# Kernel tuning notes

Hardware: AMD Instinct MI355X
Metric: run time of the kernel (lower is better)

The kernel has to match this reference:

```python
import jax, jax.numpy as jnp
import numpy as np

MU = 0.34
STD = 0.04
PATCH = 32
LOG_NORM_CONST = float(np.log(STD * np.sqrt(2.0 * np.pi)))


def _patch_means(unet_output, patch):
    # unet_output: [B, C, H, W] with B == 1 (original code implicitly requires it).
    B, C, H, W = unet_output.shape
    hp, wp = H // patch, W // patch
    x = unet_output.reshape(B * C, hp, patch, wp, patch)
    # mean over batch*channel and both intra-patch axes -> [hp, wp]
    return x.mean(axis=(0, 2, 4))


def reference(unet_output, transformer_output):
    means = _patch_means(unet_output, PATCH)              # [hp, wp]
    mask = transformer_output[0] >= 0.5                   # [hp, wp]

    # Positive branch: -log(pdf(mean) + 1e-6); original uses .item() -> detached,
    # so stop_gradient reproduces the (lack of) gradient through this branch.
    m_sg = jax.lax.stop_gradient(means)
    logpdf = -0.5 * jnp.square((m_sg - MU) / STD) - LOG_NORM_CONST
    pos_term = -jnp.log(jnp.exp(logpdf) + 1e-6)

    # Negative branch: MSE against zero = mean^2 (differentiable).
    neg_term = jnp.square(means)

    maskf = mask.astype(means.dtype)
    pos_cnt = jnp.sum(maskf)
    neg_cnt = jnp.sum(1.0 - maskf)
    positive_loss = jnp.sum(pos_term * maskf) / pos_cnt
    negative_loss = jnp.sum(neg_term * (1.0 - maskf)) / neg_cnt
    return positive_loss + negative_loss


def setup_inputs() -> dict:
    key = jax.random.key(0)
    k1, k2 = jax.random.split(key)
    unet_output = jax.random.uniform(k1, (1, 1, 8192, 8192), dtype=jnp.float32)
    transformer_output = jax.random.uniform(k2, (1, 256, 256), dtype=jnp.float32)
    return {"unet_output": unet_output, "transformer_output": transformer_output}
```

## Files before the change

### kernel.cpp

```cpp
#include <hip/hip_runtime.h>
#include <math.h>

#define IMG_H 8192
#define IMG_W 8192
#define PATCH 32
#define HP 256
#define WP 256
#define NPATCH (HP * WP)

__device__ __constant__ float c_MU  = 0.34f;
__device__ __constant__ float c_INV_STD = 25.0f;
__device__ __constant__ float c_LOG_NORM_CONST = -2.2999373f;

__global__ __launch_bounds__(256) void patch_mean_kernel(
    const float* __restrict__ x, float* __restrict__ means)
{
    const int wave  = threadIdx.x >> 6;
    const int lane  = threadIdx.x & 63;
    const int patch = blockIdx.x * 4 + wave;
    const int ph = patch >> 8;
    const int pw = patch & 255;

    const float* base = x + (size_t)(ph * PATCH) * IMG_W + (size_t)(pw * PATCH);
    const int r0 = lane >> 3;
    const int cv = lane & 7;

    float s = 0.0f;
#pragma unroll
    for (int i = 0; i < 4; ++i) {
        const float4 v = *reinterpret_cast<const float4*>(
            base + (size_t)(i * 8 + r0) * IMG_W + cv * 4);
        s += (v.x + v.y) + (v.z + v.w);
    }

#pragma unroll
    for (int off = 32; off >= 1; off >>= 1)
        s += __shfl_down(s, off, 64);

    if (lane == 0)
        means[patch] = s * (1.0f / 1024.0f);
}

__global__ __launch_bounds__(256) void loss_partial_kernel(
    const float* __restrict__ means, const float* __restrict__ tmask,
    float* __restrict__ acc)
{
    const int idx = (blockIdx.x * 256 + threadIdx.x) * 4;

    const float4 m4 = *reinterpret_cast<const float4*>(means + idx);
    const float4 t4 = *reinterpret_cast<const float4*>(tmask + idx);

    const float mv[4] = { m4.x, m4.y, m4.z, m4.w };
    const float tv[4] = { t4.x, t4.y, t4.z, t4.w };

    float pos = 0.0f, neg = 0.0f, cnt = 0.0f;
#pragma unroll
    for (int i = 0; i < 4; ++i) {
        const float z = (mv[i] - c_MU) * c_INV_STD;
        const float logpdf = -0.5f * z * z - c_LOG_NORM_CONST;
        const float pterm = -logf(expf(logpdf) + 1e-6f);
        const float nterm = mv[i] * mv[i];
        if (tv[i] >= 0.5f) { pos += pterm; cnt += 1.0f; }
        else               { neg += nterm; }
    }

#pragma unroll
    for (int off = 32; off >= 1; off >>= 1) {
        pos += __shfl_down(pos, off, 64);
        neg += __shfl_down(neg, off, 64);
        cnt += __shfl_down(cnt, off, 64);
    }

    __shared__ float s_pos[4], s_neg[4], s_cnt[4];
    const int wave = threadIdx.x >> 6;
    const int lane = threadIdx.x & 63;
    if (lane == 0) { s_pos[wave] = pos; s_neg[wave] = neg; s_cnt[wave] = cnt; }
    __syncthreads();

    if (threadIdx.x == 0) {
        float bp = s_pos[0] + s_pos[1] + s_pos[2] + s_pos[3];
        float bn = s_neg[0] + s_neg[1] + s_neg[2] + s_neg[3];
        float bc = s_cnt[0] + s_cnt[1] + s_cnt[2] + s_cnt[3];
        atomicAdd(&acc[0], bp);
        atomicAdd(&acc[1], bn);
        atomicAdd(&acc[2], bc);
    }
}

__global__ void finalize_kernel(const float* __restrict__ acc, float* __restrict__ out)
{
    const float pos_cnt = acc[2];
    const float neg_cnt = (float)NPATCH - pos_cnt;
    out[0] = acc[0] / pos_cnt + acc[1] / neg_cnt;
}

extern "C" void kernel_launch(void* const* d_in, const int* in_sizes, int n_in,
                              void* d_out, int out_size, void* d_ws, size_t ws_size,
                              hipStream_t stream)
{
    const float* unet  = (const float*)d_in[0];
    const float* trans = (const float*)d_in[1];
    float* out = (float*)d_out;

    float* means = (float*)d_ws;
    float* acc   = means + NPATCH;

    hipMemsetAsync(acc, 0, 3 * sizeof(float), stream);

    patch_mean_kernel<<<NPATCH / 4, 256, 0, stream>>>(unet, means);

    loss_partial_kernel<<<NPATCH / 1024, 256, 0, stream>>>(means, trans, acc);

    finalize_kernel<<<1, 1, 0, stream>>>(acc, out);
}
```

Measured before the change: 348.5 us.

## Fuse patch-mean and loss terms, replace atomics with single-block final reduction

The per-patch loss terms are now computed inside the patch-mean kernel, so the means array is no longer written and reread. Each block writes its partial sums to per-block slots, and a single 1024-thread kernel reduces them and computes the final loss. This drops the memset, the separate loss kernel and the atomics. The costs are an added syncthreads in the bandwidth-bound main kernel and a one-block tail reduction over 16K partials.

```diff
diff --git a/kernel.cpp b/kernel.cpp
--- a/kernel.cpp
+++ b/kernel.cpp
@@ -1,19 +1,15 @@
 #include <hip/hip_runtime.h>
 #include <math.h>
 
-#define IMG_H 8192
 #define IMG_W 8192
 #define PATCH 32
-#define HP 256
-#define WP 256
-#define NPATCH (HP * WP)
+#define NPATCH 65536
+#define NBLK   16384
 
-__device__ __constant__ float c_MU  = 0.34f;
-__device__ __constant__ float c_INV_STD = 25.0f;
-__device__ __constant__ float c_LOG_NORM_CONST = -2.2999373f;
-
-__global__ __launch_bounds__(256) void patch_mean_kernel(
-    const float* __restrict__ x, float* __restrict__ means)
+__global__ __launch_bounds__(256) void fused_patch_loss_kernel(
+    const float* __restrict__ x, const float* __restrict__ tmask,
+    float* __restrict__ p_pos, float* __restrict__ p_neg,
+    float* __restrict__ p_cnt)
 {
     const int wave  = threadIdx.x >> 6;
     const int lane  = threadIdx.x & 63;
@@ -37,31 +33,38 @@
     for (int off = 32; off >= 1; off >>= 1)
         s += __shfl_down(s, off, 64);
 
-    if (lane == 0)
-        means[patch] = s * (1.0f / 1024.0f);
+    __shared__ float s_pos[4], s_neg[4], s_cnt[4];
+    if (lane == 0) {
+        const float m = s * (1.0f / 1024.0f);
+        const float t = tmask[patch];
+        const float z = (m - 0.34f) * 25.0f;
+        const float logpdf = -0.5f * z * z + 2.2999373f;
+        const float pterm = -logf(expf(logpdf) + 1e-6f);
+        const float nterm = m * m;
+        const bool pos = (t >= 0.5f);
+        s_pos[wave] = pos ? pterm : 0.0f;
+        s_neg[wave] = pos ? 0.0f  : nterm;
+        s_cnt[wave] = pos ? 1.0f  : 0.0f;
+    }
+    __syncthreads();
+
+    if (threadIdx.x == 0) {
+        p_pos[blockIdx.x] = (s_pos[0] + s_pos[1]) + (s_pos[2] + s_pos[3]);
+        p_neg[blockIdx.x] = (s_neg[0] + s_neg[1]) + (s_neg[2] + s_neg[3]);
+        p_cnt[blockIdx.x] = (s_cnt[0] + s_cnt[1]) + (s_cnt[2] + s_cnt[3]);
+    }
 }
 
-__global__ __launch_bounds__(256) void loss_partial_kernel(
-    const float* __restrict__ means, const float* __restrict__ tmask,
-    float* __restrict__ acc)
+__global__ __launch_bounds__(1024) void finalize_reduce_kernel(
+    const float* __restrict__ p_pos, const float* __restrict__ p_neg,
+    const float* __restrict__ p_cnt, float* __restrict__ out)
 {
-    const int idx = (blockIdx.x * 256 + threadIdx.x) * 4;
-
-    const float4 m4 = *reinterpret_cast<const float4*>(means + idx);
-    const float4 t4 = *reinterpret_cast<const float4*>(tmask + idx);
-
-    const float mv[4] = { m4.x, m4.y, m4.z, m4.w };
-    const float tv[4] = { t4.x, t4.y, t4.z, t4.w };
-
     float pos = 0.0f, neg = 0.0f, cnt = 0.0f;
 #pragma unroll
-    for (int i = 0; i < 4; ++i) {
-        const float z = (mv[i] - c_MU) * c_INV_STD;
-        const float logpdf = -0.5f * z * z - c_LOG_NORM_CONST;
-        const float pterm = -logf(expf(logpdf) + 1e-6f);
-        const float nterm = mv[i] * mv[i];
-        if (tv[i] >= 0.5f) { pos += pterm; cnt += 1.0f; }
-        else               { neg += nterm; }
+    for (int i = threadIdx.x; i < NBLK; i += 1024) {
+        pos += p_pos[i];
+        neg += p_neg[i];
+        cnt += p_cnt[i];
     }
 
 #pragma unroll
@@ -71,27 +74,18 @@
         cnt += __shfl_down(cnt, off, 64);
     }
 
-    __shared__ float s_pos[4], s_neg[4], s_cnt[4];
+    __shared__ float sp[16], sn[16], sc[16];
     const int wave = threadIdx.x >> 6;
     const int lane = threadIdx.x & 63;
-    if (lane == 0) { s_pos[wave] = pos; s_neg[wave] = neg; s_cnt[wave] = cnt; }
+    if (lane == 0) { sp[wave] = pos; sn[wave] = neg; sc[wave] = cnt; }
     __syncthreads();
 
     if (threadIdx.x == 0) {
-        float bp = s_pos[0] + s_pos[1] + s_pos[2] + s_pos[3];
-        float bn = s_neg[0] + s_neg[1] + s_neg[2] + s_neg[3];
-        float bc = s_cnt[0] + s_cnt[1] + s_cnt[2] + s_cnt[3];
-        atomicAdd(&acc[0], bp);
-        atomicAdd(&acc[1], bn);
-        atomicAdd(&acc[2], bc);
+        float P = 0.0f, N = 0.0f, C = 0.0f;
+#pragma unroll
+        for (int w = 0; w < 16; ++w) { P += sp[w]; N += sn[w]; C += sc[w]; }
+        out[0] = P / C + N / ((float)NPATCH - C);
     }
-}
-
-__global__ void finalize_kernel(const float* __restrict__ acc, float* __restrict__ out)
-{
-    const float pos_cnt = acc[2];
-    const float neg_cnt = (float)NPATCH - pos_cnt;
-    out[0] = acc[0] / pos_cnt + acc[1] / neg_cnt;
 }
 
 extern "C" void kernel_launch(void* const* d_in, const int* in_sizes, int n_in,
@@ -102,14 +96,10 @@
     const float* trans = (const float*)d_in[1];
     float* out = (float*)d_out;
 
-    float* means = (float*)d_ws;
-    float* acc   = means + NPATCH;
+    float* p_pos = (float*)d_ws;
+    float* p_neg = p_pos + NBLK;
+    float* p_cnt = p_neg + NBLK;
 
-    hipMemsetAsync(acc, 0, 3 * sizeof(float), stream);
-
-    patch_mean_kernel<<<NPATCH / 4, 256, 0, stream>>>(unet, means);
-
-    loss_partial_kernel<<<NPATCH / 1024, 256, 0, stream>>>(means, trans, acc);
-
-    finalize_kernel<<<1, 1, 0, stream>>>(acc, out);
+    fused_patch_loss_kernel<<<NBLK, 256, 0, stream>>>(unet, trans, p_pos, p_neg, p_cnt);
+    finalize_reduce_kernel<<<1, 1024, 0, stream>>>(p_pos, p_neg, p_cnt, out);
 }
```

New measurement: 349.5 us. No clear change (+0.3%).
